# Optimization experiments

Measured on AMD Instinct MI355X. Metric: run time of the kernel, lower is better.

## Reference

```python
import jax, jax.numpy as jnp
import numpy as np

B, S, D = 2, 4096, 2048
HQ, HKV, HD = 16, 4, 128
W = 512  # sliding window size == block size
EPS = 1e-6


def rmsnorm(x, g):
    return x * jax.lax.rsqrt(jnp.mean(x * x, axis=-1, keepdims=True) + EPS) * g


def rope_tables(seq_len, head_dim):
    inv = 1.0 / (10000.0 ** (np.arange(0, head_dim, 2, dtype=np.float64) / head_dim))
    f = np.outer(np.arange(seq_len), inv)  # [S, HD/2]
    return jnp.asarray(np.cos(f), jnp.float32), jnp.asarray(np.sin(f), jnp.float32)


def apply_rope(x, cos, sin):
    # x: [B,S,H,HD]; interleaved even/odd rotation as in the torch module
    xe, xo = x[..., ::2], x[..., 1::2]
    c = cos[None, :, None, :]
    s = sin[None, :, None, :]
    rot = jnp.stack([xe * c - xo * s, xe * s + xo * c], axis=-1)  # [B,S,H,HD/2,2]
    return rot.reshape(x.shape)


def setup_inputs() -> dict:
    key = jax.random.key(0)
    ks = jax.random.split(key, 6)
    return {
        "x": jax.random.normal(ks[0], (B, S, D), jnp.float32),
        "g": jnp.ones((D,), jnp.float32),
        "wq": jax.random.normal(ks[1], (D, HQ * HD), jnp.float32) * 0.02,
        "wk": jax.random.normal(ks[2], (D, HKV * HD), jnp.float32) * 0.02,
        "wv": jax.random.normal(ks[3], (D, HKV * HD), jnp.float32) * 0.02,
        "wo": jax.random.normal(ks[4], (D, D), jnp.float32) * 0.02,
    }


def reference(x, g, wq, wk, wv, wo):
    xn = rmsnorm(x, g)
    q = (xn @ wq).reshape(B, S, HQ, HD)
    k = (xn @ wk).reshape(B, S, HKV, HD)
    v = (xn @ wv).reshape(B, S, HKV, HD)
    cos, sin = rope_tables(S, HD)
    q = apply_rope(q, cos, sin)
    k = apply_rope(k, cos, sin)
    # [B,H,S,HD]
    q = q.transpose(0, 2, 1, 3)
    k = k.transpose(0, 2, 1, 3)
    v = v.transpose(0, 2, 1, 3)
    # GQA: q head h reads kv head h // rep (flex_attention enable_gqa semantics)
    rep = HQ // HKV
    k = jnp.repeat(k, rep, axis=1)
    v = jnp.repeat(v, rep, axis=1)
    # Banded sliding-window attention: block i attends keys in blocks i-1 and i
    nb = S // W
    qb = q.reshape(B, HQ, nb, W, HD)
    kb = k.reshape(B, HQ, nb, W, HD)
    vb = v.reshape(B, HQ, nb, W, HD)
    zpad = jnp.zeros_like(kb[:, :, :1])
    kc = jnp.concatenate([jnp.concatenate([zpad, kb[:, :, :-1]], axis=2), kb], axis=3)  # [B,H,nb,2W,HD]
    vc = jnp.concatenate([jnp.concatenate([zpad, vb[:, :, :-1]], axis=2), vb], axis=3)
    # mask: q global = i*W+j, kv global = i*W+m-W; keep 0 <= q-kv <= W and kv>=0
    j = jnp.arange(W)[:, None]
    m = jnp.arange(2 * W)[None, :]
    rel_ok = (m >= j) & (m <= j + W)  # [W,2W]
    i = jnp.arange(nb)[:, None, None]
    valid = (i * W + m[None] - W) >= 0  # [nb,W,2W]
    mask = rel_ok[None] & valid  # [nb,W,2W]
    scale = 1.0 / np.sqrt(HD)
    scores = jnp.einsum("bhnqd,bhnkd->bhnqk", qb, kc) * scale
    scores = jnp.where(mask[None, None], scores, -jnp.inf)
    p = jax.nn.softmax(scores, axis=-1)
    out = jnp.einsum("bhnqk,bhnkd->bhnqd", p, vc)
    out = out.reshape(B, HQ, S, HD).transpose(0, 2, 1, 3).reshape(B, S, D)
    return out @ wo
```

## Files before the change

### kernel.cpp

```cpp
#include <hip/hip_runtime.h>
#include <math.h>

typedef __bf16 bf16;
typedef short  s16x8  __attribute__((ext_vector_type(8)));
typedef short  s16x4  __attribute__((ext_vector_type(4)));
typedef __bf16 bf16x4 __attribute__((ext_vector_type(4)));
typedef __bf16 bf16x2 __attribute__((ext_vector_type(2)));
typedef float  f32x4  __attribute__((ext_vector_type(4)));

constexpr int CB = 2, CS = 4096, CD = 2048, CHQ = 16, CHKV = 4, CHD = 128, CW = 512;
constexpr int CM = CB * CS;

#define MFMA32(a, b, c) __builtin_amdgcn_mfma_f32_16x16x32_bf16((a), (b), (c), 0, 0, 0)

#if defined(__has_builtin)
#if __has_builtin(__builtin_amdgcn_mfma_f32_16x16x16bf16_1k)
#define HAVE_MFMA16_1K 1
#endif
#endif

static __device__ __forceinline__ f32x4 MFMA16(s16x4 a, s16x4 b, f32x4 c) {
#ifdef HAVE_MFMA16_1K
  return __builtin_amdgcn_mfma_f32_16x16x16bf16_1k(a, b, c, 0, 0, 0);
#else
  asm volatile("v_mfma_f32_16x16x16_bf16 %0, %1, %2, %0" : "+v"(c) : "v"(a), "v"(b));
  return c;
#endif
}

__global__ __launch_bounds__(256) void k_rmsnorm(const float* __restrict__ x,
                                                 const float* __restrict__ g,
                                                 bf16* __restrict__ xn) {
  const int row = blockIdx.x;
  const int tid = threadIdx.x;
  const float* xr = x + (size_t)row * CD;
  float4 v0 = *(const float4*)(xr + tid * 4);
  float4 v1 = *(const float4*)(xr + tid * 4 + 1024);
  float ss = v0.x * v0.x + v0.y * v0.y + v0.z * v0.z + v0.w * v0.w
           + v1.x * v1.x + v1.y * v1.y + v1.z * v1.z + v1.w * v1.w;
#pragma unroll
  for (int o = 1; o < 64; o <<= 1) ss += __shfl_xor(ss, o);
  __shared__ float red[4];
  if ((tid & 63) == 0) red[tid >> 6] = ss;
  __syncthreads();
  float tot = red[0] + red[1] + red[2] + red[3];
  float inv = rsqrtf(tot * (1.0f / CD) + 1e-6f);
  float4 g0 = *(const float4*)(g + tid * 4);
  float4 g1 = *(const float4*)(g + tid * 4 + 1024);
  bf16x4 o0, o1;
  o0[0] = (bf16)(v0.x * inv * g0.x); o0[1] = (bf16)(v0.y * inv * g0.y);
  o0[2] = (bf16)(v0.z * inv * g0.z); o0[3] = (bf16)(v0.w * inv * g0.w);
  o1[0] = (bf16)(v1.x * inv * g1.x); o1[1] = (bf16)(v1.y * inv * g1.y);
  o1[2] = (bf16)(v1.z * inv * g1.z); o1[3] = (bf16)(v1.w * inv * g1.w);
  *(bf16x4*)(xn + (size_t)row * CD + tid * 4) = o0;
  *(bf16x4*)(xn + (size_t)row * CD + tid * 4 + 1024) = o1;
}

__global__ __launch_bounds__(256) void k_transpose(const float* __restrict__ Wsrc,
                                                   bf16* __restrict__ Wt,
                                                   int K, int N) {
  __shared__ float tile[32][33];
  const int tx = threadIdx.x & 31, ty = threadIdx.x >> 5;
  const int c0 = blockIdx.x * 32, r0 = blockIdx.y * 32;
#pragma unroll
  for (int i = 0; i < 32; i += 8)
    tile[ty + i][tx] = Wsrc[(size_t)(r0 + ty + i) * N + c0 + tx];
  __syncthreads();
#pragma unroll
  for (int i = 0; i < 32; i += 8)
    Wt[(size_t)(c0 + ty + i) * K + r0 + tx] = (bf16)tile[tx][ty + i];
}

__global__ void k_rope_inv(double* __restrict__ inv) {
  int i = threadIdx.x;
  if (i < 64) inv[i] = pow(10000.0, -(double)i / 64.0);
}

__global__ __launch_bounds__(256) void k_rope_tables(const double* __restrict__ inv,
                                                     float* __restrict__ cosT,
                                                     float* __restrict__ sinT) {
  int idx = blockIdx.x * 256 + threadIdx.x;
  int s = idx >> 6, i = idx & 63;
  double f = (double)s * inv[i];
  double n = floor(f * 0.15915494309189535 + 0.5);
  float r = (float)(f - n * 6.283185307179586);
  cosT[idx] = cosf(r);
  sinT[idx] = sinf(r);
}

__global__ __launch_bounds__(256) void k_rope(bf16* __restrict__ qk,
                                              const float* __restrict__ cosT,
                                              const float* __restrict__ sinT,
                                              int lognh) {
  size_t idx = (size_t)blockIdx.x * 256 + threadIdx.x;
  int i = (int)(idx & 63);
  int s = (int)((idx >> (6 + lognh)) & (CS - 1));
  bf16x2 p = *(bf16x2*)(qk + 2 * idx);
  float xe = (float)p[0], xo = (float)p[1];
  float c = cosT[s * 64 + i], sn = sinT[s * 64 + i];
  bf16x2 o;
  o[0] = (bf16)(xe * c - xo * sn);
  o[1] = (bf16)(xe * sn + xo * c);
  *(bf16x2*)(qk + 2 * idx) = o;
}

constexpr int BM = 128, BN = 128, BK = 64;

template <int EPI>
__global__ __launch_bounds__(256)
void k_gemm(const bf16* __restrict__ A, const bf16* __restrict__ Bt,
            void* __restrict__ Cp, int M, int N, int K) {
  __shared__ alignas(16) bf16 As[BM * BK];
  __shared__ alignas(16) bf16 Bs[BN * BK];
  const int tid = threadIdx.x;
  const int wave = tid >> 6;
  const int lane = tid & 63;
  const int bn0 = blockIdx.x * BN;
  const int bm0 = blockIdx.y * BM;
  const int wm = wave >> 1, wn = wave & 1;

  int segBase[4], srcOff[4];
#pragma unroll
  for (int i = 0; i < 4; ++i) {
    int o = ((i * 4 + wave) << 10) + lane * 16;
    int r = o >> 7;
    int cb = (o & 127) ^ ((r & 7) << 4);
    segBase[i] = (i * 4 + wave) << 10;
    srcOff[i] = r * (K * 2) + cb;
  }
  const char* Abase = (const char*)A + (size_t)bm0 * (K * 2);
  const char* Bbase = (const char*)Bt + (size_t)bn0 * (K * 2);
  char* AsB = (char*)As;
  char* BsB = (char*)Bs;

  f32x4 acc[4][4];
#pragma unroll
  for (int i = 0; i < 4; ++i)
#pragma unroll
    for (int j = 0; j < 4; ++j) acc[i][j] = (f32x4){0.f, 0.f, 0.f, 0.f};

  const int nkt = K >> 6;
  for (int kt = 0; kt < nkt; ++kt) {
#pragma unroll
    for (int i = 0; i < 4; ++i)
      __builtin_amdgcn_global_load_lds(
          (const __attribute__((address_space(1))) void*)(Abase + srcOff[i] + kt * 128),
          (__attribute__((address_space(3))) void*)(AsB + segBase[i]), 16, 0, 0);
#pragma unroll
    for (int i = 0; i < 4; ++i)
      __builtin_amdgcn_global_load_lds(
          (const __attribute__((address_space(1))) void*)(Bbase + srcOff[i] + kt * 128),
          (__attribute__((address_space(3))) void*)(BsB + segBase[i]), 16, 0, 0);
    __syncthreads();
#pragma unroll
    for (int kk = 0; kk < 2; ++kk) {
      s16x8 af[4], bfv[4];
#pragma unroll
      for (int i = 0; i < 4; ++i) {
        int row = wm * 64 + i * 16 + (lane & 15);
        int cb = ((kk * 64) + ((lane >> 4) * 16)) ^ ((row & 7) << 4);
        af[i] = *(const s16x8*)(AsB + row * 128 + cb);
        int rowb = wn * 64 + i * 16 + (lane & 15);
        int cbb = ((kk * 64) + ((lane >> 4) * 16)) ^ ((rowb & 7) << 4);
        bfv[i] = *(const s16x8*)(BsB + rowb * 128 + cbb);
      }
#pragma unroll
      for (int i = 0; i < 4; ++i)
#pragma unroll
        for (int j = 0; j < 4; ++j)
          acc[i][j] = MFMA32(af[i], bfv[j], acc[i][j]);
    }
    __syncthreads();
  }

  const int lr = (lane >> 4) * 4;
  const int lc = lane & 15;
  if constexpr (EPI == 2) {
    bf16* C = (bf16*)Cp;
#pragma unroll
    for (int i = 0; i < 4; ++i)
#pragma unroll
      for (int j = 0; j < 4; ++j) {
        int n = bn0 + wn * 64 + j * 16 + lc;
        int kvh = n >> 7, d = n & 127;
        int m = bm0 + wm * 64 + i * 16 + lr;
        int b = m >> 12, s0i = m & (CS - 1);
        bf16x4 pk;
        pk[0] = (bf16)acc[i][j][0]; pk[1] = (bf16)acc[i][j][1];
        pk[2] = (bf16)acc[i][j][2]; pk[3] = (bf16)acc[i][j][3];
        *(bf16x4*)(C + (((size_t)b * CHKV + kvh) * CHD + d) * CS + s0i) = pk;
      }
  } else if constexpr (EPI == 3) {
    bf16* C = (bf16*)Cp;
#pragma unroll
    for (int i = 0; i < 4; ++i)
#pragma unroll
      for (int j = 0; j < 4; ++j) {
        int n = bn0 + wn * 64 + j * 16 + lc;
        int kvh = n >> 7, d = n & 127;
        int m = bm0 + wm * 64 + i * 16 + lr;
        int b = m >> 12, s0i = m & (CS - 1);
#pragma unroll
        for (int r = 0; r < 4; ++r)
          C[(((size_t)b * CHKV + kvh) * CS + (s0i + r)) * CHD + d] = (bf16)acc[i][j][r];
      }
  } else {
#pragma unroll
    for (int i = 0; i < 4; ++i)
#pragma unroll
      for (int j = 0; j < 4; ++j) {
        int n = bn0 + wn * 64 + j * 16 + lc;
        int m = bm0 + wm * 64 + i * 16 + lr;
#pragma unroll
        for (int r = 0; r < 4; ++r) {
          if constexpr (EPI == 0)
            ((float*)Cp)[(size_t)(m + r) * N + n] = acc[i][j][r];
          else
            ((bf16*)Cp)[(size_t)(m + r) * N + n] = (bf16)acc[i][j][r];
        }
      }
  }
}

__global__ __launch_bounds__(256) void k_attn(const bf16* __restrict__ Q,
                                              const bf16* __restrict__ Kb,
                                              const bf16* __restrict__ Vt,
                                              bf16* __restrict__ O) {
  __shared__ alignas(16) char lds[2][16384];
  int blk = (int)blockIdx.x;
  blk = (blk & 7) * 128 + (blk >> 3);
  const int qt = blk & 127;
  const int kv = (blk >> 7) & 3;
  const int b  = blk >> 9;
  const int tid = threadIdx.x;
  const int lane = tid & 63, wv = tid >> 6;
  const int g = lane >> 4, qi = lane & 15;
  const int h = kv * 4 + wv;
  const int q0 = qt * 32;
  const float SCL2 = 0.1275174308f;

  s16x8 qf[2][4];
#pragma unroll
  for (int sub = 0; sub < 2; ++sub) {
    const bf16* qb_ = Q + (((size_t)b * CS + q0 + sub * 16 + qi) * CHQ + h) * CHD + g * 8;
#pragma unroll
    for (int t = 0; t < 4; ++t) qf[sub][t] = *(const s16x8*)(qb_ + t * 32);
  }

  f32x4 ot[2][8];
#pragma unroll
  for (int sub = 0; sub < 2; ++sub)
#pragma unroll
    for (int t = 0; t < 8; ++t) ot[sub][t] = (f32x4){0.f, 0.f, 0.f, 0.f};
  float m_run[2] = {-__builtin_inff(), -__builtin_inff()};
  float l_run[2] = {0.f, 0.f};

  const int kstart = (q0 >= CW) ? (q0 - CW) : 0;
  const int nc = (q0 + 32 - kstart) >> 5;

  const char* Kbase = (const char*)Kb + (size_t)(b * CHKV + kv) * CS * 256;
  const char* Vbase = (const char*)Vt + (size_t)(b * CHKV + kv) * CHD * (CS * 2);

  const int krow = tid >> 4;
  const int kcol = (tid & 15) * 16;
  const int ksw0 = krow * 256 + (kcol ^ ((krow & 7) << 4));
  const int ksw1 = (krow + 16) * 256 + (kcol ^ ((krow & 7) << 4));
  const int vrow = tid >> 2;
  const int vcol = (tid & 3) * 16;
  const size_t vsw0 = (size_t)vrow * (CS * 2) + (vcol ^ ((vrow & 3) << 4));
  const size_t vsw1 = (size_t)(vrow + 64) * (CS * 2) + (vcol ^ ((vrow & 3) << 4));

#define STAGE(kc_, buf_) do {                                                   \
    const char* kS_ = Kbase + (size_t)(kc_) * 256;                              \
    const char* vS_ = Vbase + (size_t)(kc_) * 2;                                \
    char* d_ = (char*)lds[buf_];                                                \
    __builtin_amdgcn_global_load_lds(                                           \
        (const __attribute__((address_space(1))) void*)(kS_ + ksw0),            \
        (__attribute__((address_space(3))) void*)(d_ + wv * 1024), 16, 0, 0);   \
    __builtin_amdgcn_global_load_lds(                                           \
        (const __attribute__((address_space(1))) void*)(kS_ + ksw1),            \
        (__attribute__((address_space(3))) void*)(d_ + 4096 + wv * 1024), 16, 0, 0); \
    __builtin_amdgcn_global_load_lds(                                           \
        (const __attribute__((address_space(1))) void*)(vS_ + vsw0),            \
        (__attribute__((address_space(3))) void*)(d_ + 8192 + wv * 1024), 16, 0, 0); \
    __builtin_amdgcn_global_load_lds(                                           \
        (const __attribute__((address_space(1))) void*)(vS_ + vsw1),            \
        (__attribute__((address_space(3))) void*)(d_ + 12288 + wv * 1024), 16, 0, 0); \
  } while (0)

  STAGE(kstart, 0);
  __syncthreads();
  int cur = 0;

  for (int c = 0; c < nc; ++c) {
    const int kc = kstart + c * 32;
    if (c + 1 < nc) STAGE(kc + 32, cur ^ 1);

    const char* KL = (const char*)lds[cur];
    const char* VL = (const char*)lds[cur] + 8192;

    f32x4 sc[2][2];
    sc[0][0] = (f32x4){0.f,0.f,0.f,0.f}; sc[0][1] = (f32x4){0.f,0.f,0.f,0.f};
    sc[1][0] = (f32x4){0.f,0.f,0.f,0.f}; sc[1][1] = (f32x4){0.f,0.f,0.f,0.f};
    __builtin_amdgcn_s_setprio(1);
#pragma unroll
    for (int t = 0; t < 4; ++t) {
      const int co = (t * 64 + g * 16) ^ ((qi & 7) << 4);
      s16x8 k0 = *(const s16x8*)(KL + qi * 256 + co);
      s16x8 k1 = *(const s16x8*)(KL + 4096 + qi * 256 + co);
      sc[0][0] = MFMA32(k0, qf[0][t], sc[0][0]);
      sc[0][1] = MFMA32(k1, qf[0][t], sc[0][1]);
      sc[1][0] = MFMA32(k0, qf[1][t], sc[1][0]);
      sc[1][1] = MFMA32(k1, qf[1][t], sc[1][1]);
    }
    __builtin_amdgcn_s_setprio(0);

    s16x4 pb[2][2];
#pragma unroll
    for (int sub = 0; sub < 2; ++sub) {
      const int qg = q0 + sub * 16 + qi;
      float p[8];
#pragma unroll
      for (int hf = 0; hf < 2; ++hf)
#pragma unroll
        for (int r = 0; r < 4; ++r) {
          int key = kc + hf * 16 + g * 4 + r;
          float v = sc[sub][hf][r] * SCL2;
          p[hf * 4 + r] = (key <= qg && key + CW >= qg) ? v : -__builtin_inff();
        }
      float pm = fmaxf(fmaxf(fmaxf(p[0], p[1]), fmaxf(p[2], p[3])),
                       fmaxf(fmaxf(p[4], p[5]), fmaxf(p[6], p[7])));
      pm = fmaxf(pm, __shfl_xor(pm, 16));
      pm = fmaxf(pm, __shfl_xor(pm, 32));
      if (__any(pm - m_run[sub] > 11.5f)) {
        float mn = fmaxf(m_run[sub], pm);
        float fs = exp2f(m_run[sub] - mn);
        l_run[sub] *= fs;
#pragma unroll
        for (int t = 0; t < 8; ++t) {
          ot[sub][t][0] *= fs; ot[sub][t][1] *= fs;
          ot[sub][t][2] *= fs; ot[sub][t][3] *= fs;
        }
        m_run[sub] = mn;
      }
      float rs = 0.f;
#pragma unroll
      for (int i2 = 0; i2 < 8; ++i2) { p[i2] = exp2f(p[i2] - m_run[sub]); rs += p[i2]; }
      rs += __shfl_xor(rs, 16);
      rs += __shfl_xor(rs, 32);
      l_run[sub] += rs;
#pragma unroll
      for (int j = 0; j < 4; ++j) {
        pb[sub][0][j] = __builtin_bit_cast(short, (bf16)p[j]);
        pb[sub][1][j] = __builtin_bit_cast(short, (bf16)p[4 + j]);
      }
    }

    __builtin_amdgcn_s_setprio(1);
#pragma unroll
    for (int t = 0; t < 8; ++t) {
      const int rowd = t * 16 + qi;
      const int sw = (rowd & 3) << 4;
      s16x4 v0 = *(const s16x4*)(VL + rowd * 64 + ((g * 8) ^ sw));
      s16x4 v1 = *(const s16x4*)(VL + rowd * 64 + ((32 + g * 8) ^ sw));
      ot[0][t] = MFMA16(v0, pb[0][0], ot[0][t]);
      ot[0][t] = MFMA16(v1, pb[0][1], ot[0][t]);
      ot[1][t] = MFMA16(v0, pb[1][0], ot[1][t]);
      ot[1][t] = MFMA16(v1, pb[1][1], ot[1][t]);
    }
    __builtin_amdgcn_s_setprio(0);

    __syncthreads();
    cur ^= 1;
  }
#undef STAGE

#pragma unroll
  for (int sub = 0; sub < 2; ++sub) {
    float invl = 1.0f / l_run[sub];
    bf16* ob = O + (((size_t)b * CS + q0 + sub * 16 + qi) * CHQ + h) * CHD;
#pragma unroll
    for (int t = 0; t < 8; ++t) {
      bf16x4 pk;
      pk[0] = (bf16)(ot[sub][t][0] * invl);
      pk[1] = (bf16)(ot[sub][t][1] * invl);
      pk[2] = (bf16)(ot[sub][t][2] * invl);
      pk[3] = (bf16)(ot[sub][t][3] * invl);
      *(bf16x4*)(ob + t * 16 + g * 4) = pk;
    }
  }
}

extern "C" void kernel_launch(void* const* d_in, const int* in_sizes, int n_in,
                              void* d_out, int out_size, void* d_ws, size_t ws_size,
                              hipStream_t stream) {
  const float* x = (const float*)d_in[0];
  const float* g = (const float*)d_in[1];
  const float* wq = (const float*)d_in[2];
  const float* wk = (const float*)d_in[3];
  const float* wv = (const float*)d_in[4];
  const float* wo = (const float*)d_in[5];
  float* out = (float*)d_out;

  char* p = (char*)d_ws;
  bf16* xn = (bf16*)p;  p += (size_t)CM * CD * 2;
  bf16* wqT = (bf16*)p; p += (size_t)CD * CD * 2;
  bf16* wkT = (bf16*)p; p += (size_t)(CHKV * CHD) * CD * 2;
  bf16* wvT = (bf16*)p; p += (size_t)(CHKV * CHD) * CD * 2;
  bf16* woT = (bf16*)p; p += (size_t)CD * CD * 2;
  double* invT = (double*)p; p += 64 * 8;
  float* cosT = (float*)p; p += (size_t)CS * 64 * 4;
  float* sinT = (float*)p; p += (size_t)CS * 64 * 4;
  bf16* qb = (bf16*)p;  p += (size_t)CM * CD * 2;
  bf16* kb = (bf16*)p;  p += (size_t)CM * (CHKV * CHD) * 2;
  bf16* vT = (bf16*)p;  p += (size_t)CM * (CHKV * CHD) * 2;
  bf16* ao = xn;

  k_rope_inv<<<1, 64, 0, stream>>>(invT);
  k_rope_tables<<<(CS * 64) / 256, 256, 0, stream>>>(invT, cosT, sinT);
  k_rmsnorm<<<CM, 256, 0, stream>>>(x, g, xn);
  k_transpose<<<dim3(CD / 32, CD / 32), 256, 0, stream>>>(wq, wqT, CD, CD);
  k_transpose<<<dim3((CHKV * CHD) / 32, CD / 32), 256, 0, stream>>>(wk, wkT, CD, CHKV * CHD);
  k_transpose<<<dim3((CHKV * CHD) / 32, CD / 32), 256, 0, stream>>>(wv, wvT, CD, CHKV * CHD);
  k_transpose<<<dim3(CD / 32, CD / 32), 256, 0, stream>>>(wo, woT, CD, CD);

  k_gemm<1><<<dim3(CD / BN, CM / BM), 256, 0, stream>>>(xn, wqT, qb, CM, CD, CD);
  k_gemm<3><<<dim3((CHKV * CHD) / BN, CM / BM), 256, 0, stream>>>(xn, wkT, kb, CM, CHKV * CHD, CD);
  k_gemm<2><<<dim3((CHKV * CHD) / BN, CM / BM), 256, 0, stream>>>(xn, wvT, vT, CM, CHKV * CHD, CD);

  k_rope<<<(CM * CHQ * 64) / 256, 256, 0, stream>>>(qb, cosT, sinT, 4);
  k_rope<<<(CM * CHKV * 64) / 256, 256, 0, stream>>>(kb, cosT, sinT, 0);

  k_attn<<<CB * CHKV * (CS / 32), 256, 0, stream>>>(qb, kb, vT, ao);

  k_gemm<0><<<dim3(CD / BN, CM / BM), 256, 0, stream>>>(ao, woT, out, CM, CD, CD);
}
```

Baseline: 538.1 us.

## Fuse QKV projections into one GEMM, batch transposes and rope, skip interior masking

Concatenates the Q, K and V weight transposes into one buffer and runs a single GEMM whose epilogue routes column ranges to the Q, K and V-transposed layouts. The four transposes become one launch, and the two rope launches become one. In attention, the mask comparisons run only for key chunks near the window edges, and the V LDS layout and swizzle are changed to pack two d-rows per 128-element line. This cuts launch count and tail waste and raises GEMM grid occupancy, at the cost of more complex indexing and epilogue branching.

```diff
diff --git a/kernel.cpp b/kernel.cpp
--- a/kernel.cpp
+++ b/kernel.cpp
@@ -56,19 +56,28 @@
   *(bf16x4*)(xn + (size_t)row * CD + tid * 4 + 1024) = o1;
 }
 
-__global__ __launch_bounds__(256) void k_transpose(const float* __restrict__ Wsrc,
-                                                   bf16* __restrict__ Wt,
-                                                   int K, int N) {
+__global__ __launch_bounds__(256) void k_transpose_all(
+    const float* __restrict__ wq, const float* __restrict__ wk,
+    const float* __restrict__ wv, const float* __restrict__ wo,
+    bf16* __restrict__ wqkvT, bf16* __restrict__ woT) {
   __shared__ float tile[32][33];
+  int bid = blockIdx.x;
+  const float* src; bf16* dst; int N_;
+  if (bid < 4096)      { src = wq; dst = wqkvT;                          N_ = 2048; }
+  else if (bid < 5120) { src = wk; dst = wqkvT + (size_t)2048 * 2048;    N_ = 512;  bid -= 4096; }
+  else if (bid < 6144) { src = wv; dst = wqkvT + (size_t)2560 * 2048;    N_ = 512;  bid -= 5120; }
+  else                 { src = wo; dst = woT;                            N_ = 2048; bid -= 6144; }
+  const int ntx = N_ >> 5;
+  const int bx = bid & (ntx - 1), by = bid / ntx;
   const int tx = threadIdx.x & 31, ty = threadIdx.x >> 5;
-  const int c0 = blockIdx.x * 32, r0 = blockIdx.y * 32;
+  const int c0 = bx * 32, r0 = by * 32;
 #pragma unroll
   for (int i = 0; i < 32; i += 8)
-    tile[ty + i][tx] = Wsrc[(size_t)(r0 + ty + i) * N + c0 + tx];
+    tile[ty + i][tx] = src[(size_t)(r0 + ty + i) * N_ + c0 + tx];
   __syncthreads();
 #pragma unroll
   for (int i = 0; i < 32; i += 8)
-    Wt[(size_t)(c0 + ty + i) * K + r0 + tx] = (bf16)tile[tx][ty + i];
+    dst[(size_t)(c0 + ty + i) * 2048 + r0 + tx] = (bf16)tile[tx][ty + i];
 }
 
 __global__ void k_rope_inv(double* __restrict__ inv) {
@@ -88,20 +97,26 @@
   sinT[idx] = sinf(r);
 }
 
-__global__ __launch_bounds__(256) void k_rope(bf16* __restrict__ qk,
-                                              const float* __restrict__ cosT,
-                                              const float* __restrict__ sinT,
-                                              int lognh) {
+constexpr size_t NQP = (size_t)CM * CHQ * 64;
+__global__ __launch_bounds__(256) void k_rope2(bf16* __restrict__ qb,
+                                               bf16* __restrict__ kb,
+                                               const float* __restrict__ cosT,
+                                               const float* __restrict__ sinT) {
   size_t idx = (size_t)blockIdx.x * 256 + threadIdx.x;
-  int i = (int)(idx & 63);
-  int s = (int)((idx >> (6 + lognh)) & (CS - 1));
-  bf16x2 p = *(bf16x2*)(qk + 2 * idx);
+  bf16* ptr; int s, i;
+  if (idx < NQP) {
+    i = (int)(idx & 63); s = (int)((idx >> 10) & (CS - 1)); ptr = qb + 2 * idx;
+  } else {
+    size_t j = idx - NQP;
+    i = (int)(j & 63); s = (int)((j >> 6) & (CS - 1)); ptr = kb + 2 * j;
+  }
+  bf16x2 p = *(bf16x2*)ptr;
   float xe = (float)p[0], xo = (float)p[1];
   float c = cosT[s * 64 + i], sn = sinT[s * 64 + i];
   bf16x2 o;
   o[0] = (bf16)(xe * c - xo * sn);
   o[1] = (bf16)(xe * sn + xo * c);
-  *(bf16x2*)(qk + 2 * idx) = o;
+  *(bf16x2*)ptr = o;
 }
 
 constexpr int BM = 128, BN = 128, BK = 64;
@@ -109,7 +124,8 @@
 template <int EPI>
 __global__ __launch_bounds__(256)
 void k_gemm(const bf16* __restrict__ A, const bf16* __restrict__ Bt,
-            void* __restrict__ Cp, int M, int N, int K) {
+            void* __restrict__ Cp, bf16* __restrict__ Ck, bf16* __restrict__ Cv,
+            int M, int N, int K) {
   __shared__ alignas(16) bf16 As[BM * BK];
   __shared__ alignas(16) bf16 Bs[BN * BK];
   const int tid = threadIdx.x;
@@ -175,35 +191,47 @@
 
   const int lr = (lane >> 4) * 4;
   const int lc = lane & 15;
-  if constexpr (EPI == 2) {
-    bf16* C = (bf16*)Cp;
-#pragma unroll
-    for (int i = 0; i < 4; ++i)
-#pragma unroll
-      for (int j = 0; j < 4; ++j) {
-        int n = bn0 + wn * 64 + j * 16 + lc;
-        int kvh = n >> 7, d = n & 127;
-        int m = bm0 + wm * 64 + i * 16 + lr;
-        int b = m >> 12, s0i = m & (CS - 1);
-        bf16x4 pk;
-        pk[0] = (bf16)acc[i][j][0]; pk[1] = (bf16)acc[i][j][1];
-        pk[2] = (bf16)acc[i][j][2]; pk[3] = (bf16)acc[i][j][3];
-        *(bf16x4*)(C + (((size_t)b * CHKV + kvh) * CHD + d) * CS + s0i) = pk;
-      }
-  } else if constexpr (EPI == 3) {
-    bf16* C = (bf16*)Cp;
-#pragma unroll
-    for (int i = 0; i < 4; ++i)
-#pragma unroll
-      for (int j = 0; j < 4; ++j) {
-        int n = bn0 + wn * 64 + j * 16 + lc;
-        int kvh = n >> 7, d = n & 127;
-        int m = bm0 + wm * 64 + i * 16 + lr;
-        int b = m >> 12, s0i = m & (CS - 1);
-#pragma unroll
-        for (int r = 0; r < 4; ++r)
-          C[(((size_t)b * CHKV + kvh) * CS + (s0i + r)) * CHD + d] = (bf16)acc[i][j][r];
-      }
+  if constexpr (EPI == 4) {
+    if (bn0 < 2048) {
+      bf16* C = (bf16*)Cp;
+#pragma unroll
+      for (int i = 0; i < 4; ++i)
+#pragma unroll
+        for (int j = 0; j < 4; ++j) {
+          int n = bn0 + wn * 64 + j * 16 + lc;
+          int m = bm0 + wm * 64 + i * 16 + lr;
+#pragma unroll
+          for (int r = 0; r < 4; ++r)
+            C[(size_t)(m + r) * 2048 + n] = (bf16)acc[i][j][r];
+        }
+    } else if (bn0 < 2560) {
+#pragma unroll
+      for (int i = 0; i < 4; ++i)
+#pragma unroll
+        for (int j = 0; j < 4; ++j) {
+          int n = bn0 - 2048 + wn * 64 + j * 16 + lc;
+          int kvh = n >> 7, d = n & 127;
+          int m = bm0 + wm * 64 + i * 16 + lr;
+          int b = m >> 12, s0i = m & (CS - 1);
+#pragma unroll
+          for (int r = 0; r < 4; ++r)
+            Ck[(((size_t)b * CHKV + kvh) * CS + (s0i + r)) * CHD + d] = (bf16)acc[i][j][r];
+        }
+    } else {
+#pragma unroll
+      for (int i = 0; i < 4; ++i)
+#pragma unroll
+        for (int j = 0; j < 4; ++j) {
+          int n = bn0 - 2560 + wn * 64 + j * 16 + lc;
+          int kvh = n >> 7, d = n & 127;
+          int m = bm0 + wm * 64 + i * 16 + lr;
+          int b = m >> 12, s0i = m & (CS - 1);
+          bf16x4 pk;
+          pk[0] = (bf16)acc[i][j][0]; pk[1] = (bf16)acc[i][j][1];
+          pk[2] = (bf16)acc[i][j][2]; pk[3] = (bf16)acc[i][j][3];
+          *(bf16x4*)(Cv + (((size_t)b * CHKV + kvh) * CHD + d) * CS + s0i) = pk;
+        }
+    }
   } else {
 #pragma unroll
     for (int i = 0; i < 4; ++i)
@@ -212,12 +240,8 @@
         int n = bn0 + wn * 64 + j * 16 + lc;
         int m = bm0 + wm * 64 + i * 16 + lr;
 #pragma unroll
-        for (int r = 0; r < 4; ++r) {
-          if constexpr (EPI == 0)
-            ((float*)Cp)[(size_t)(m + r) * N + n] = acc[i][j][r];
-          else
-            ((bf16*)Cp)[(size_t)(m + r) * N + n] = (bf16)acc[i][j][r];
-        }
+        for (int r = 0; r < 4; ++r)
+          ((float*)Cp)[(size_t)(m + r) * N + n] = acc[i][j][r];
       }
   }
 }
@@ -265,10 +289,11 @@
   const int kcol = (tid & 15) * 16;
   const int ksw0 = krow * 256 + (kcol ^ ((krow & 7) << 4));
   const int ksw1 = (krow + 16) * 256 + (kcol ^ ((krow & 7) << 4));
-  const int vrow = tid >> 2;
-  const int vcol = (tid & 3) * 16;
-  const size_t vsw0 = (size_t)vrow * (CS * 2) + (vcol ^ ((vrow & 3) << 4));
-  const size_t vsw1 = (size_t)(vrow + 64) * (CS * 2) + (vcol ^ ((vrow & 3) << 4));
+  const int vA = tid * 16;
+  const int vr0 = vA >> 7;
+  const int vL = (vA & 127) ^ ((vr0 & 7) << 4);
+  const size_t vsw0 = (size_t)(2 * vr0 + (vL >> 6)) * (CS * 2) + (vL & 63);
+  const size_t vsw1 = vsw0 + (size_t)64 * (CS * 2);
 
 #define STAGE(kc_, buf_) do {                                                   \
     const char* kS_ = Kbase + (size_t)(kc_) * 256;                              \
@@ -315,19 +340,29 @@
     }
     __builtin_amdgcn_s_setprio(0);
 
+    const bool edge = (kc + 31 > q0) || (kc + 481 < q0);
+
     s16x4 pb[2][2];
 #pragma unroll
     for (int sub = 0; sub < 2; ++sub) {
       const int qg = q0 + sub * 16 + qi;
       float p[8];
-#pragma unroll
-      for (int hf = 0; hf < 2; ++hf)
-#pragma unroll
-        for (int r = 0; r < 4; ++r) {
-          int key = kc + hf * 16 + g * 4 + r;
-          float v = sc[sub][hf][r] * SCL2;
-          p[hf * 4 + r] = (key <= qg && key + CW >= qg) ? v : -__builtin_inff();
-        }
+      if (edge) {
+#pragma unroll
+        for (int hf = 0; hf < 2; ++hf)
+#pragma unroll
+          for (int r = 0; r < 4; ++r) {
+            int key = kc + hf * 16 + g * 4 + r;
+            float v = sc[sub][hf][r] * SCL2;
+            p[hf * 4 + r] = (key <= qg && key + CW >= qg) ? v : -__builtin_inff();
+          }
+      } else {
+#pragma unroll
+        for (int hf = 0; hf < 2; ++hf)
+#pragma unroll
+          for (int r = 0; r < 4; ++r)
+            p[hf * 4 + r] = sc[sub][hf][r] * SCL2;
+      }
       float pm = fmaxf(fmaxf(fmaxf(p[0], p[1]), fmaxf(p[2], p[3])),
                        fmaxf(fmaxf(p[4], p[5]), fmaxf(p[6], p[7])));
       pm = fmaxf(pm, __shfl_xor(pm, 16));
@@ -360,9 +395,12 @@
 #pragma unroll
     for (int t = 0; t < 8; ++t) {
       const int rowd = t * 16 + qi;
-      const int sw = (rowd & 3) << 4;
-      s16x4 v0 = *(const s16x4*)(VL + rowd * 64 + ((g * 8) ^ sw));
-      s16x4 v1 = *(const s16x4*)(VL + rowd * 64 + ((32 + g * 8) ^ sw));
+      const int vr_ = rowd >> 1;
+      const int base = vr_ * 128;
+      const int dsel = (rowd & 1) << 6;
+      const int sw = (vr_ & 7) << 4;
+      s16x4 v0 = *(const s16x4*)(VL + base + ((dsel + g * 8) ^ sw));
+      s16x4 v1 = *(const s16x4*)(VL + base + ((dsel + 32 + g * 8) ^ sw));
       ot[0][t] = MFMA16(v0, pb[0][0], ot[0][t]);
       ot[0][t] = MFMA16(v1, pb[0][1], ot[0][t]);
       ot[1][t] = MFMA16(v0, pb[1][0], ot[1][t]);
@@ -403,12 +441,10 @@
   float* out = (float*)d_out;
 
   char* p = (char*)d_ws;
-  bf16* xn = (bf16*)p;  p += (size_t)CM * CD * 2;
-  bf16* wqT = (bf16*)p; p += (size_t)CD * CD * 2;
-  bf16* wkT = (bf16*)p; p += (size_t)(CHKV * CHD) * CD * 2;
-  bf16* wvT = (bf16*)p; p += (size_t)(CHKV * CHD) * CD * 2;
-  bf16* woT = (bf16*)p; p += (size_t)CD * CD * 2;
-  double* invT = (double*)p; p += 64 * 8;
+  bf16* xn = (bf16*)p;    p += (size_t)CM * CD * 2;
+  bf16* wqkvT = (bf16*)p; p += (size_t)3072 * CD * 2;
+  bf16* woT = (bf16*)p;   p += (size_t)CD * CD * 2;
+  double* invT = (double*)p; p += 4096;
   float* cosT = (float*)p; p += (size_t)CS * 64 * 4;
   float* sinT = (float*)p; p += (size_t)CS * 64 * 4;
   bf16* qb = (bf16*)p;  p += (size_t)CM * CD * 2;
@@ -419,19 +455,15 @@
   k_rope_inv<<<1, 64, 0, stream>>>(invT);
   k_rope_tables<<<(CS * 64) / 256, 256, 0, stream>>>(invT, cosT, sinT);
   k_rmsnorm<<<CM, 256, 0, stream>>>(x, g, xn);
-  k_transpose<<<dim3(CD / 32, CD / 32), 256, 0, stream>>>(wq, wqT, CD, CD);
-  k_transpose<<<dim3((CHKV * CHD) / 32, CD / 32), 256, 0, stream>>>(wk, wkT, CD, CHKV * CHD);
-  k_transpose<<<dim3((CHKV * CHD) / 32, CD / 32), 256, 0, stream>>>(wv, wvT, CD, CHKV * CHD);
-  k_transpose<<<dim3(CD / 32, CD / 32), 256, 0, stream>>>(wo, woT, CD, CD);
-
-  k_gemm<1><<<dim3(CD / BN, CM / BM), 256, 0, stream>>>(xn, wqT, qb, CM, CD, CD);
-  k_gemm<3><<<dim3((CHKV * CHD) / BN, CM / BM), 256, 0, stream>>>(xn, wkT, kb, CM, CHKV * CHD, CD);
-  k_gemm<2><<<dim3((CHKV * CHD) / BN, CM / BM), 256, 0, stream>>>(xn, wvT, vT, CM, CHKV * CHD, CD);
-
-  k_rope<<<(CM * CHQ * 64) / 256, 256, 0, stream>>>(qb, cosT, sinT, 4);
-  k_rope<<<(CM * CHKV * 64) / 256, 256, 0, stream>>>(kb, cosT, sinT, 0);
+  k_transpose_all<<<10240, 256, 0, stream>>>(wq, wk, wv, wo, wqkvT, woT);
+
+  k_gemm<4><<<dim3(3072 / BN, CM / BM), 256, 0, stream>>>(xn, wqkvT, qb, kb, vT,
+                                                          CM, 3072, CD);
+
+  k_rope2<<<(int)((NQP + (size_t)CM * CHKV * 64) / 256), 256, 0, stream>>>(qb, kb, cosT, sinT);
 
   k_attn<<<CB * CHKV * (CS / 32), 256, 0, stream>>>(qb, kb, vT, ao);
 
-  k_gemm<0><<<dim3(CD / BN, CM / BM), 256, 0, stream>>>(ao, woT, out, CM, CD, CD);
-}
+  k_gemm<0><<<dim3(CD / BN, CM / BM), 256, 0, stream>>>(ao, woT, out, nullptr, nullptr,
+                                                        CM, CD, CD);
+}
```

New measurement: 460.8 us. -14.4%, faster.
